# Kernel optimization log

Measured on AMD Instinct MI355X. Metric: run time of the kernel, lower is better.

The kernel has to match this reference:

```python
import jax, jax.numpy as jnp
import numpy as np
import math

B, T, C, H = 2, 2048, 1024, 16

def setup_inputs() -> dict:
    key = jax.random.key(0)
    ks = jax.random.split(key, 5)
    s = 0.02
    return {
        "x": jax.random.normal(ks[0], (B, T, C), dtype=jnp.float32),
        "W_attn": jax.random.normal(ks[1], (C, 3 * C), dtype=jnp.float32) * s,
        "b_attn": jnp.zeros((3 * C,), dtype=jnp.float32),
        "W_proj": jax.random.normal(ks[2], (C, C), dtype=jnp.float32) * s,
        "b_proj": jnp.zeros((C,), dtype=jnp.float32),
    }

def reference(x, W_attn, b_attn, W_proj, b_proj):
    Bx, Tx, Cx = x.shape
    hd = Cx // H  # head dim = 64
    qkv = x @ W_attn + b_attn                      # [B,T,3C]
    q, k, v = jnp.split(qkv, 3, axis=-1)
    # [B,H,T,hd]
    q = q.reshape(Bx, Tx, H, hd).transpose(0, 2, 1, 3)
    k = k.reshape(Bx, Tx, H, hd).transpose(0, 2, 1, 3)
    v = v.reshape(Bx, Tx, H, hd).transpose(0, 2, 1, 3)
    scale = 1.0 / math.sqrt(hd)
    att = jnp.einsum('bhqd,bhkd->bhqk', q, k) * scale   # [B,H,T,T]
    causal = jnp.tril(jnp.ones((Tx, Tx), dtype=bool))
    att = jnp.where(causal[None, None, :, :], att, -jnp.inf)
    att = jax.nn.softmax(att, axis=-1)
    y = jnp.einsum('bhqk,bhkd->bhqd', att, v)           # [B,H,T,hd]
    y = y.transpose(0, 2, 1, 3).reshape(Bx, Tx, Cx)
    return y @ W_proj + b_proj
```

## Files before the change

### kernel.cpp

```cpp
#include <hip/hip_runtime.h>

typedef __attribute__((ext_vector_type(8))) __bf16 bf16x8;
typedef __attribute__((ext_vector_type(4))) float f32x4;

#define T_SEQ 2048
#define NH 16
#define HD 64
#define CDIM 1024
#define NQK 2048
#define NQKV 3072
#define MTOT 4096

#define SWZ(r, c) ((((r) * 8) + ((c) ^ ((r) & 7))) * 8)

__device__ __forceinline__ void async_load16(const void* g, void* l) {
    __builtin_amdgcn_global_load_lds(
        (const __attribute__((address_space(1))) void*)g,
        (__attribute__((address_space(3))) void*)l, 16, 0, 0);
}

__global__ __launch_bounds__(256) void cvt_bf16_kernel(const float* __restrict__ in,
                                                       __bf16* __restrict__ out, int n) {
    int i = (blockIdx.x * 256 + threadIdx.x) * 8;
    if (i + 8 <= n) {
        float4 f0 = *(const float4*)(in + i);
        float4 f1 = *(const float4*)(in + i + 4);
        bf16x8 o;
        o[0] = (__bf16)f0.x; o[1] = (__bf16)f0.y; o[2] = (__bf16)f0.z; o[3] = (__bf16)f0.w;
        o[4] = (__bf16)f1.x; o[5] = (__bf16)f1.y; o[6] = (__bf16)f1.z; o[7] = (__bf16)f1.w;
        *(bf16x8*)(out + i) = o;
    }
}

__global__ __launch_bounds__(256) void transpose2_kernel(
    const float* __restrict__ Wa, const float* __restrict__ Wp,
    __bf16* __restrict__ WaT, __bf16* __restrict__ WpT) {
    __shared__ float tile[32][33];
    const float* in; __bf16* out; int C, bx = blockIdx.x;
    if (bx < 96) { in = Wa; out = WaT; C = 3072; }
    else         { in = Wp; out = WpT; C = 1024; bx -= 96; }
    int c0 = bx * 32, r0 = blockIdx.y * 32;
    int tx = threadIdx.x, ty = threadIdx.y;
#pragma unroll
    for (int i = 0; i < 4; i++)
        tile[ty + i * 8][tx] = in[(size_t)(r0 + ty + i * 8) * C + c0 + tx];
    __syncthreads();
#pragma unroll
    for (int i = 0; i < 4; i++)
        out[(size_t)(c0 + ty + i * 8) * 1024 + r0 + tx] = (__bf16)tile[tx][ty + i * 8];
}

template <int WNW>
__global__ __launch_bounds__(256) void gemm_bt_kernel(
    const __bf16* __restrict__ A, const __bf16* __restrict__ Bt,
    const float* __restrict__ bias, int M, int N, int K, int mode,
    __bf16* __restrict__ qkb, __bf16* __restrict__ vtb, float* __restrict__ outf)
{
    constexpr int MI = (WNW == 2) ? 4 : 2;
    constexpr int BROWS = WNW * 64;
    __shared__ __bf16 As[128 * 64];
    __shared__ __bf16 Bs[BROWS * 64];

    int tid = threadIdx.x;
    int lane = tid & 63, wid = tid >> 6;
    int quad = lane >> 4, r16 = lane & 15;
    int wm = (WNW == 2) ? (wid >> 1) * 64 : wid * 32;
    int wn = (WNW == 2) ? (wid & 1) * 64 : 0;
    int bm = blockIdx.y * 128, bn = blockIdx.x * (WNW * 64);

    f32x4 acc[MI][4] = {};

    int lrow = lane >> 3;
    int lcolsw = (((lane & 7) ^ (lrow & 7)) * 8);
    const __bf16* Ag = A + (size_t)(bm + wid * 32 + lrow) * K + lcolsw;
    const __bf16* Bg = Bt + (size_t)(bn + wid * (BROWS / 4) + lrow) * K + lcolsw;
    char* lA = (char*)As + wid * 4096;
    char* lB = (char*)Bs + wid * (BROWS / 4) * 128;

    for (int kt = 0; kt < K; kt += 64) {
        __syncthreads();
#pragma unroll
        for (int i = 0; i < 4; i++)
            async_load16(Ag + kt + (size_t)i * 8 * K, lA + i * 1024);
#pragma unroll
        for (int i = 0; i < BROWS / 32; i++)
            async_load16(Bg + kt + (size_t)i * 8 * K, lB + i * 1024);
        __syncthreads();
#pragma unroll
        for (int ks = 0; ks < 2; ks++) {
            bf16x8 af[MI], bfr[4];
#pragma unroll
            for (int i = 0; i < MI; i++)
                af[i] = *(const bf16x8*)&As[SWZ(wm + i * 16 + r16, ks * 4 + quad)];
#pragma unroll
            for (int i = 0; i < 4; i++)
                bfr[i] = *(const bf16x8*)&Bs[SWZ(wn + i * 16 + r16, ks * 4 + quad)];
#pragma unroll
            for (int mi = 0; mi < MI; mi++)
#pragma unroll
                for (int ni = 0; ni < 4; ni++)
                    acc[mi][ni] = __builtin_amdgcn_mfma_f32_16x16x32_bf16(
                        af[mi], bfr[ni], acc[mi][ni], 0, 0, 0);
        }
    }

    const float SC2 = 0.125f * 1.44269504088896f;
#pragma unroll
    for (int mi = 0; mi < MI; mi++) {
#pragma unroll
        for (int ni = 0; ni < 4; ni++) {
            int col = bn + wn + ni * 16 + r16;
            float bv = bias[col];
            int row0 = bm + wm + mi * 16 + quad * 4;
            if (mode == 1) {
#pragma unroll
                for (int rg = 0; rg < 4; rg++)
                    outf[(size_t)(row0 + rg) * N + col] = acc[mi][ni][rg] + bv;
            } else if (col < 1024) {
#pragma unroll
                for (int rg = 0; rg < 4; rg++)
                    qkb[(size_t)(row0 + rg) * NQK + col] = (__bf16)((acc[mi][ni][rg] + bv) * SC2);
            } else if (col < 2048) {
#pragma unroll
                for (int rg = 0; rg < 4; rg++)
                    qkb[(size_t)(row0 + rg) * NQK + col] = (__bf16)(acc[mi][ni][rg] + bv);
            } else {
                int dcol = col - 2048;
                int b = row0 >> 11, t0 = row0 & 2047;
                union { __bf16 h[4]; uint2 u; } pk;
#pragma unroll
                for (int rg = 0; rg < 4; rg++) pk.h[rg] = (__bf16)(acc[mi][ni][rg] + bv);
                *(uint2*)&vtb[((size_t)b * 1024 + dcol) * T_SEQ + t0] = pk.u;
            }
        }
    }
}

__global__ __launch_bounds__(256) void attn_kernel(
    const __bf16* __restrict__ qkb, const __bf16* __restrict__ vtb,
    __bf16* __restrict__ y1)
{
    __shared__ __bf16 Ks[64 * 64];
    __shared__ __bf16 Vs[64 * 64];
    __shared__ __bf16 Ps[4][32][72];

    int tid = threadIdx.x;
    int lane = tid & 63, w = tid >> 6;
    int quad = lane >> 4, r16 = lane & 15;
    int bh = blockIdx.y;
    int b = bh >> 4, h = bh & 15;
    int qtA = blockIdx.x, qtB = 31 - qtA;
    int qbA = qtA * 64, qbB = qtB * 64;

    const __bf16* Qh = qkb + (size_t)b * T_SEQ * NQK + h * HD;
    const __bf16* Kh = Qh + CDIM;
    const __bf16* Vh = vtb + ((size_t)b * 1024 + h * HD) * T_SEQ;

    const float NEG_INF = -__builtin_inff();
    int lrow = lane >> 3;
    int lcolsw = (((lane & 7) ^ (lrow & 7)) * 8);
    char* lK = (char*)Ks + w * 2048;
    char* lV = (char*)Vs + w * 2048;

    bf16x8 qfA[2], qfB[2];
#pragma unroll
    for (int ks = 0; ks < 2; ks++) {
        qfA[ks] = *(const bf16x8*)(Qh + (size_t)(qbA + w * 16 + r16) * NQK + ks * 32 + quad * 8);
        qfB[ks] = *(const bf16x8*)(Qh + (size_t)(qbB + w * 16 + r16) * NQK + ks * 32 + quad * 8);
    }
    f32x4 oA[4] = {}, oB[4] = {};
    float lA_ = 0.f, lB_ = 0.f;
    int g0A = qbA + w * 16, g0B = qbB + w * 16;
    int qrowA = g0A + r16, qrowB = g0B + r16;

    int nktA = qtA + 1, nktB = qtB + 1;
    for (int kt = 0; kt < nktB; kt++) {
        int kb = kt * 64;
        __syncthreads();
        const __bf16* kg = Kh + (size_t)(kb + w * 16 + lrow) * NQK + lcolsw;
        const __bf16* vg = Vh + (size_t)(w * 16 + lrow) * T_SEQ + kb + lcolsw;
        async_load16(kg, lK);
        async_load16(kg + (size_t)8 * NQK, lK + 1024);
        async_load16(vg, lV);
        async_load16(vg + (size_t)8 * T_SEQ, lV + 1024);
        __syncthreads();

        bool doA = (kt < nktA);

        f32x4 sB[4] = {}, sA[4] = {};
#pragma unroll
        for (int ks = 0; ks < 2; ks++) {
            bf16x8 kf[4];
#pragma unroll
            for (int ni = 0; ni < 4; ni++)
                kf[ni] = *(const bf16x8*)&Ks[SWZ(ni * 16 + r16, ks * 4 + quad)];
#pragma unroll
            for (int ni = 0; ni < 4; ni++)
                sB[ni] = __builtin_amdgcn_mfma_f32_16x16x32_bf16(kf[ni], qfB[ks], sB[ni], 0, 0, 0);
            if (doA) {
#pragma unroll
                for (int ni = 0; ni < 4; ni++)
                    sA[ni] = __builtin_amdgcn_mfma_f32_16x16x32_bf16(kf[ni], qfA[ks], sA[ni], 0, 0, 0);
            }
        }
        if (kb + 63 > g0B) {
#pragma unroll
            for (int ni = 0; ni < 4; ni++)
#pragma unroll
                for (int rg = 0; rg < 4; rg++)
                    if (kb + ni * 16 + quad * 4 + rg > qrowB) sB[ni][rg] = NEG_INF;
        }
#pragma unroll
        for (int ni = 0; ni < 4; ni++) {
            union { __bf16 h[4]; uint2 u; } pk;
#pragma unroll
            for (int rg = 0; rg < 4; rg++) {
                float p = exp2f(sB[ni][rg]);
                lB_ += p;
                pk.h[rg] = (__bf16)p;
            }
            *(uint2*)&Ps[w][r16][ni * 16 + quad * 4] = pk.u;
        }
        if (doA) {
            if (kb + 63 > g0A) {
#pragma unroll
                for (int ni = 0; ni < 4; ni++)
#pragma unroll
                    for (int rg = 0; rg < 4; rg++)
                        if (kb + ni * 16 + quad * 4 + rg > qrowA) sA[ni][rg] = NEG_INF;
            }
#pragma unroll
            for (int ni = 0; ni < 4; ni++) {
                union { __bf16 h[4]; uint2 u; } pk;
#pragma unroll
                for (int rg = 0; rg < 4; rg++) {
                    float p = exp2f(sA[ni][rg]);
                    lA_ += p;
                    pk.h[rg] = (__bf16)p;
                }
                *(uint2*)&Ps[w][16 + r16][ni * 16 + quad * 4] = pk.u;
            }
        }
#pragma unroll
        for (int ks = 0; ks < 2; ks++) {
            bf16x8 vf[4];
#pragma unroll
            for (int nd = 0; nd < 4; nd++)
                vf[nd] = *(const bf16x8*)&Vs[SWZ(nd * 16 + r16, ks * 4 + quad)];
            bf16x8 pbB = *(const bf16x8*)&Ps[w][r16][ks * 32 + quad * 8];
#pragma unroll
            for (int nd = 0; nd < 4; nd++)
                oB[nd] = __builtin_amdgcn_mfma_f32_16x16x32_bf16(vf[nd], pbB, oB[nd], 0, 0, 0);
            if (doA) {
                bf16x8 pbA = *(const bf16x8*)&Ps[w][16 + r16][ks * 32 + quad * 8];
#pragma unroll
                for (int nd = 0; nd < 4; nd++)
                    oA[nd] = __builtin_amdgcn_mfma_f32_16x16x32_bf16(vf[nd], pbA, oA[nd], 0, 0, 0);
            }
        }
    }

#pragma unroll
    for (int which = 0; which < 2; which++) {
        f32x4* o = which ? oB : oA;
        float rs = which ? lB_ : lA_;
        rs += __shfl_xor(rs, 16, 64);
        rs += __shfl_xor(rs, 32, 64);
        float inv = 1.f / rs;
        int t = (which ? qbB : qbA) + w * 16 + r16;
#pragma unroll
        for (int nd = 0; nd < 4; nd++) {
            union { __bf16 h[4]; uint2 u; } pk;
#pragma unroll
            for (int rg = 0; rg < 4; rg++) pk.h[rg] = (__bf16)(o[nd][rg] * inv);
            *(uint2*)&y1[(size_t)(b * T_SEQ + t) * CDIM + h * HD + nd * 16 + quad * 4] = pk.u;
        }
    }
}

extern "C" void kernel_launch(void* const* d_in, const int* in_sizes, int n_in,
                              void* d_out, int out_size, void* d_ws, size_t ws_size,
                              hipStream_t stream) {
    const float* x = (const float*)d_in[0];
    const float* W_attn = (const float*)d_in[1];
    const float* b_attn = (const float*)d_in[2];
    const float* W_proj = (const float*)d_in[3];
    const float* b_proj = (const float*)d_in[4];
    float* out = (float*)d_out;

    char* p = (char*)d_ws;
    __bf16* xb = (__bf16*)p;   p += (size_t)MTOT * CDIM * 2;
    __bf16* WaT = (__bf16*)p;  p += (size_t)3 * CDIM * CDIM * 2;
    __bf16* WpT = (__bf16*)p;  p += (size_t)CDIM * CDIM * 2;
    __bf16* qkb = (__bf16*)p;  p += (size_t)MTOT * NQK * 2;
    __bf16* vtb = (__bf16*)p;  p += (size_t)2 * 1024 * T_SEQ * 2;
    __bf16* y1 = xb;

    cvt_bf16_kernel<<<2048, 256, 0, stream>>>(x, xb, MTOT * CDIM);
    transpose2_kernel<<<dim3(128, 32), dim3(32, 8), 0, stream>>>(W_attn, W_proj, WaT, WpT);
    gemm_bt_kernel<2><<<dim3(24, 32), 256, 0, stream>>>(xb, WaT, b_attn, MTOT, NQKV, CDIM, 0,
                                                        qkb, vtb, nullptr);
    attn_kernel<<<dim3(16, 32), 256, 0, stream>>>(qkb, vtb, y1);
    gemm_bt_kernel<1><<<dim3(16, 32), 256, 0, stream>>>(y1, WpT, b_proj, MTOT, CDIM, CDIM, 1,
                                                        nullptr, nullptr, out);
}
```

Baseline: 190.1 us.

## Load 128-key K/V tiles per barrier in attention and swap GEMM grid order

The attention kernel now stages 128 keys of K and V per iteration and processes them as two 64-key sub-blocks. This halves the number of __syncthreads pairs and load phases per head, at the cost of more LDS per block (K and V buffers doubled) and a new swizzle for the wider V tile. Separately, the GEMM grids swap the x/y block mapping so that consecutive blocks walk along M rather than N, which changes L2 reuse of the weight tiles.

```diff
diff --git a/kernel.cpp b/kernel.cpp
--- a/kernel.cpp
+++ b/kernel.cpp
@@ -12,6 +12,7 @@
 #define MTOT 4096
 
 #define SWZ(r, c) ((((r) * 8) + ((c) ^ ((r) & 7))) * 8)
+#define SWZV(r, g) ((((r) * 16) + (((g) & 8) | (((g) & 7) ^ ((r) & 7)))) * 8)
 
 __device__ __forceinline__ void async_load16(const void* g, void* l) {
     __builtin_amdgcn_global_load_lds(
@@ -66,7 +67,7 @@
     int quad = lane >> 4, r16 = lane & 15;
     int wm = (WNW == 2) ? (wid >> 1) * 64 : wid * 32;
     int wn = (WNW == 2) ? (wid & 1) * 64 : 0;
-    int bm = blockIdx.y * 128, bn = blockIdx.x * (WNW * 64);
+    int bm = blockIdx.x * 128, bn = blockIdx.y * (WNW * 64);
 
     f32x4 acc[MI][4] = {};
 
@@ -140,8 +141,8 @@
     const __bf16* __restrict__ qkb, const __bf16* __restrict__ vtb,
     __bf16* __restrict__ y1)
 {
-    __shared__ __bf16 Ks[64 * 64];
-    __shared__ __bf16 Vs[64 * 64];
+    __shared__ __bf16 Ks[128 * 64];
+    __shared__ __bf16 Vs[64 * 128];
     __shared__ __bf16 Ps[4][32][72];
 
     int tid = threadIdx.x;
@@ -157,10 +158,10 @@
     const __bf16* Vh = vtb + ((size_t)b * 1024 + h * HD) * T_SEQ;
 
     const float NEG_INF = -__builtin_inff();
-    int lrow = lane >> 3;
-    int lcolsw = (((lane & 7) ^ (lrow & 7)) * 8);
-    char* lK = (char*)Ks + w * 2048;
-    char* lV = (char*)Vs + w * 2048;
+    int ks_lrow = lane >> 3, ks_s = lane & 7;
+    int vs_lrow = lane >> 4, vs_s = lane & 15;
+    char* lKb = (char*)Ks + w * 32 * 128;
+    char* lVb = (char*)Vs + w * 16 * 256;
 
     bf16x8 qfA[2], qfB[2];
 #pragma unroll
@@ -174,88 +175,98 @@
     int qrowA = g0A + r16, qrowB = g0B + r16;
 
     int nktA = qtA + 1, nktB = qtB + 1;
-    for (int kt = 0; kt < nktB; kt++) {
-        int kb = kt * 64;
+    int nst = (nktB + 1) >> 1;
+    for (int st = 0; st < nst; st++) {
+        int kb = st * 128;
         __syncthreads();
-        const __bf16* kg = Kh + (size_t)(kb + w * 16 + lrow) * NQK + lcolsw;
-        const __bf16* vg = Vh + (size_t)(w * 16 + lrow) * T_SEQ + kb + lcolsw;
-        async_load16(kg, lK);
-        async_load16(kg + (size_t)8 * NQK, lK + 1024);
-        async_load16(vg, lV);
-        async_load16(vg + (size_t)8 * T_SEQ, lV + 1024);
+#pragma unroll
+        for (int i = 0; i < 4; i++) {
+            int krow = w * 32 + i * 8 + ks_lrow;
+            async_load16(Kh + (size_t)(kb + krow) * NQK + (ks_s ^ (krow & 7)) * 8,
+                         lKb + i * 1024);
+            int drow = w * 16 + i * 4 + vs_lrow;
+            int vg = (vs_s & 8) | ((vs_s & 7) ^ (drow & 7));
+            async_load16(Vh + (size_t)drow * T_SEQ + kb + vg * 8, lVb + i * 1024);
+        }
         __syncthreads();
 
-        bool doA = (kt < nktA);
-
-        f32x4 sB[4] = {}, sA[4] = {};
-#pragma unroll
-        for (int ks = 0; ks < 2; ks++) {
-            bf16x8 kf[4];
-#pragma unroll
-            for (int ni = 0; ni < 4; ni++)
-                kf[ni] = *(const bf16x8*)&Ks[SWZ(ni * 16 + r16, ks * 4 + quad)];
-#pragma unroll
-            for (int ni = 0; ni < 4; ni++)
-                sB[ni] = __builtin_amdgcn_mfma_f32_16x16x32_bf16(kf[ni], qfB[ks], sB[ni], 0, 0, 0);
-            if (doA) {
+#pragma unroll
+        for (int sub = 0; sub < 2; sub++) {
+            int kidx = st * 2 + sub;
+            if (kidx >= nktB) break;
+            int kbs = kb + sub * 64;
+            bool doA = (kidx < nktA);
+
+            f32x4 sB[4] = {}, sA[4] = {};
+#pragma unroll
+            for (int ks = 0; ks < 2; ks++) {
+                bf16x8 kf[4];
 #pragma unroll
                 for (int ni = 0; ni < 4; ni++)
-                    sA[ni] = __builtin_amdgcn_mfma_f32_16x16x32_bf16(kf[ni], qfA[ks], sA[ni], 0, 0, 0);
-            }
-        }
-        if (kb + 63 > g0B) {
-#pragma unroll
-            for (int ni = 0; ni < 4; ni++)
-#pragma unroll
-                for (int rg = 0; rg < 4; rg++)
-                    if (kb + ni * 16 + quad * 4 + rg > qrowB) sB[ni][rg] = NEG_INF;
-        }
-#pragma unroll
-        for (int ni = 0; ni < 4; ni++) {
-            union { __bf16 h[4]; uint2 u; } pk;
-#pragma unroll
-            for (int rg = 0; rg < 4; rg++) {
-                float p = exp2f(sB[ni][rg]);
-                lB_ += p;
-                pk.h[rg] = (__bf16)p;
-            }
-            *(uint2*)&Ps[w][r16][ni * 16 + quad * 4] = pk.u;
-        }
-        if (doA) {
-            if (kb + 63 > g0A) {
+                    kf[ni] = *(const bf16x8*)&Ks[SWZ(sub * 64 + ni * 16 + r16, ks * 4 + quad)];
 #pragma unroll
                 for (int ni = 0; ni < 4; ni++)
+                    sB[ni] = __builtin_amdgcn_mfma_f32_16x16x32_bf16(kf[ni], qfB[ks], sB[ni], 0, 0, 0);
+                if (doA) {
+#pragma unroll
+                    for (int ni = 0; ni < 4; ni++)
+                        sA[ni] = __builtin_amdgcn_mfma_f32_16x16x32_bf16(kf[ni], qfA[ks], sA[ni], 0, 0, 0);
+                }
+            }
+            if (kbs + 63 > g0B) {
+#pragma unroll
+                for (int ni = 0; ni < 4; ni++)
 #pragma unroll
                     for (int rg = 0; rg < 4; rg++)
-                        if (kb + ni * 16 + quad * 4 + rg > qrowA) sA[ni][rg] = NEG_INF;
+                        if (kbs + ni * 16 + quad * 4 + rg > qrowB) sB[ni][rg] = NEG_INF;
             }
 #pragma unroll
             for (int ni = 0; ni < 4; ni++) {
                 union { __bf16 h[4]; uint2 u; } pk;
 #pragma unroll
                 for (int rg = 0; rg < 4; rg++) {
-                    float p = exp2f(sA[ni][rg]);
-                    lA_ += p;
+                    float p = exp2f(sB[ni][rg]);
+                    lB_ += p;
                     pk.h[rg] = (__bf16)p;
                 }
-                *(uint2*)&Ps[w][16 + r16][ni * 16 + quad * 4] = pk.u;
-            }
-        }
-#pragma unroll
-        for (int ks = 0; ks < 2; ks++) {
-            bf16x8 vf[4];
-#pragma unroll
-            for (int nd = 0; nd < 4; nd++)
-                vf[nd] = *(const bf16x8*)&Vs[SWZ(nd * 16 + r16, ks * 4 + quad)];
-            bf16x8 pbB = *(const bf16x8*)&Ps[w][r16][ks * 32 + quad * 8];
-#pragma unroll
-            for (int nd = 0; nd < 4; nd++)
-                oB[nd] = __builtin_amdgcn_mfma_f32_16x16x32_bf16(vf[nd], pbB, oB[nd], 0, 0, 0);
+                *(uint2*)&Ps[w][r16][ni * 16 + quad * 4] = pk.u;
+            }
             if (doA) {
-                bf16x8 pbA = *(const bf16x8*)&Ps[w][16 + r16][ks * 32 + quad * 8];
+                if (kbs + 63 > g0A) {
+#pragma unroll
+                    for (int ni = 0; ni < 4; ni++)
+#pragma unroll
+                        for (int rg = 0; rg < 4; rg++)
+                            if (kbs + ni * 16 + quad * 4 + rg > qrowA) sA[ni][rg] = NEG_INF;
+                }
+#pragma unroll
+                for (int ni = 0; ni < 4; ni++) {
+                    union { __bf16 h[4]; uint2 u; } pk;
+#pragma unroll
+                    for (int rg = 0; rg < 4; rg++) {
+                        float p = exp2f(sA[ni][rg]);
+                        lA_ += p;
+                        pk.h[rg] = (__bf16)p;
+                    }
+                    *(uint2*)&Ps[w][16 + r16][ni * 16 + quad * 4] = pk.u;
+                }
+            }
+#pragma unroll
+            for (int ks = 0; ks < 2; ks++) {
+                bf16x8 vf[4];
 #pragma unroll
                 for (int nd = 0; nd < 4; nd++)
-                    oA[nd] = __builtin_amdgcn_mfma_f32_16x16x32_bf16(vf[nd], pbA, oA[nd], 0, 0, 0);
+                    vf[nd] = *(const bf16x8*)&Vs[SWZV(nd * 16 + r16, sub * 8 + ks * 4 + quad)];
+                bf16x8 pbB = *(const bf16x8*)&Ps[w][r16][ks * 32 + quad * 8];
+#pragma unroll
+                for (int nd = 0; nd < 4; nd++)
+                    oB[nd] = __builtin_amdgcn_mfma_f32_16x16x32_bf16(vf[nd], pbB, oB[nd], 0, 0, 0);
+                if (doA) {
+                    bf16x8 pbA = *(const bf16x8*)&Ps[w][16 + r16][ks * 32 + quad * 8];
+#pragma unroll
+                    for (int nd = 0; nd < 4; nd++)
+                        oA[nd] = __builtin_amdgcn_mfma_f32_16x16x32_bf16(vf[nd], pbA, oA[nd], 0, 0, 0);
+                }
             }
         }
     }
@@ -298,9 +309,9 @@
 
     cvt_bf16_kernel<<<2048, 256, 0, stream>>>(x, xb, MTOT * CDIM);
     transpose2_kernel<<<dim3(128, 32), dim3(32, 8), 0, stream>>>(W_attn, W_proj, WaT, WpT);
-    gemm_bt_kernel<2><<<dim3(24, 32), 256, 0, stream>>>(xb, WaT, b_attn, MTOT, NQKV, CDIM, 0,
+    gemm_bt_kernel<2><<<dim3(32, 24), 256, 0, stream>>>(xb, WaT, b_attn, MTOT, NQKV, CDIM, 0,
                                                         qkb, vtb, nullptr);
     attn_kernel<<<dim3(16, 32), 256, 0, stream>>>(qkb, vtb, y1);
-    gemm_bt_kernel<1><<<dim3(16, 32), 256, 0, stream>>>(y1, WpT, b_proj, MTOT, CDIM, CDIM, 1,
+    gemm_bt_kernel<1><<<dim3(32, 16), 256, 0, stream>>>(y1, WpT, b_proj, MTOT, CDIM, CDIM, 1,
                                                         nullptr, nullptr, out);
 }
```

Result: no change. 187.1 us (-1.6%).
